# Optimization experiments

Measured on AMD Instinct MI355X. Metric: run time of the kernel, lower is better.

The kernel has to match this reference:

```python
import jax, jax.numpy as jnp
import numpy as np

N_NODES = 10000
N_EDGES = 100000
IN_CH = 64
EDGE_DIM = 16
HID = 128
HEADS = 4
LAYERS = 4
NUM_GRAPHS = 256


def setup_inputs() -> dict:
    key = jax.random.key(0)
    ks = jax.random.split(key, 16)
    s = 0.1
    HC = HEADS * HID
    L = LAYERS
    return {
        "x": jax.random.normal(ks[0], (N_NODES, IN_CH), jnp.float32),
        "edge_index": jax.random.randint(ks[1], (2, N_EDGES), 0, N_NODES, dtype=jnp.int32),
        "edge_attr": jax.random.normal(ks[2], (N_EDGES, EDGE_DIM), jnp.float32),
        "batch": jnp.sort(jax.random.randint(ks[3], (N_NODES,), 0, NUM_GRAPHS, dtype=jnp.int32)),
        "Win": jax.random.normal(ks[4], (IN_CH, HID), jnp.float32) * s,
        "b_in": jnp.zeros((HID,), jnp.float32),
        "Wl": jax.random.normal(ks[5], (L, HID, HC), jnp.float32) * s,
        "bl": jnp.zeros((L, HC), jnp.float32),
        "Wr": jax.random.normal(ks[6], (L, HID, HC), jnp.float32) * s,
        "br": jnp.zeros((L, HC), jnp.float32),
        "We": jax.random.normal(ks[7], (L, EDGE_DIM, HC), jnp.float32) * s,
        "att": jax.random.normal(ks[8], (L, HEADS, HID), jnp.float32) * s,
        "b_gat": jnp.zeros((L, HID), jnp.float32),
        "gamma": jnp.ones((L, HID), jnp.float32),
        "beta": jnp.zeros((L, HID), jnp.float32),
        "Wres": jax.random.normal(ks[9], (L - 1, HID, HID), jnp.float32) * s,
        "bres": jnp.zeros((L - 1, HID), jnp.float32),
        "W1": jax.random.normal(ks[10], (HID, HID), jnp.float32) * s,
        "b1": jnp.zeros((HID,), jnp.float32),
        "W2": jax.random.normal(ks[11], (HID, HID // 2), jnp.float32) * s,
        "b2": jnp.zeros((HID // 2,), jnp.float32),
        "W3": jax.random.normal(ks[12], (HID // 2, 1), jnp.float32) * s,
        "b3": jnp.zeros((1,), jnp.float32),
    }


def _layer_norm(x, g, b):
    mu = x.mean(-1, keepdims=True)
    var = ((x - mu) ** 2).mean(-1, keepdims=True)
    return g * (x - mu) / jnp.sqrt(var + 1e-5) + b


def _gatv2(h, src, dst, edge_attr, Wl, bl, Wr, br, We, att, bias):
    # GATv2Conv, concat=False, share_weights=False, negative_slope=0.2, eval mode
    N = h.shape[0]
    H, C = att.shape
    xl = (h @ Wl + bl).reshape(N, H, C)   # source-side features (lin_l)
    xr = (h @ Wr + br).reshape(N, H, C)   # target-side features (lin_r)
    e = (edge_attr @ We).reshape(-1, H, C)
    m = xl[src] + xr[dst] + e             # [E, H, C]
    m = jnp.where(m > 0, m, 0.2 * m)      # leaky_relu
    logits = jnp.einsum('ehc,hc->eh', m, att)
    lmax = jax.lax.stop_gradient(jax.ops.segment_max(logits, dst, num_segments=N))
    p = jnp.exp(logits - lmax[dst])
    denom = jax.ops.segment_sum(p, dst, num_segments=N)
    alpha = p / (denom[dst] + 1e-16)      # segment softmax over in-edges of each target
    out = jax.ops.segment_sum(alpha[:, :, None] * xl[src], dst, num_segments=N)
    return out.mean(axis=1) + bias        # concat=False -> head mean, plus bias


def reference(x, edge_index, edge_attr, batch, Win, b_in, Wl, bl, Wr, br, We, att,
              b_gat, gamma, beta, Wres, bres, W1, b1, W2, b2, W3, b3):
    src, dst = edge_index[0], edge_index[1]
    h = jax.nn.elu(x @ Win + b_in)
    for i in range(LAYERS):
        h_res = h
        h = _gatv2(h, src, dst, edge_attr, Wl[i], bl[i], Wr[i], br[i], We[i], att[i], b_gat[i])
        h = jax.nn.elu(_layer_norm(h, gamma[i], beta[i]))
        if i > 0:
            h = h + (h_res @ Wres[i - 1] + bres[i - 1])
    sums = jax.ops.segment_sum(h, batch, num_segments=NUM_GRAPHS)
    counts = jax.ops.segment_sum(jnp.ones((h.shape[0], 1), h.dtype), batch, num_segments=NUM_GRAPHS)
    hg = sums / jnp.maximum(counts, 1.0)  # global_mean_pool
    z = jax.nn.relu(hg @ W1 + b1)
    z = jax.nn.relu(z @ W2 + b2)
    return (z @ W3 + b3).reshape(-1)
```

## Files before the change

kernel.cpp:

```cpp
#include <hip/hip_runtime.h>

#define N_NODES 10000
#define N_EDGES 100000
#define IN_CH 64
#define EDGE_DIM 16
#define HID 128
#define HEADS 4
#define HC 512
#define LAYERS 4
#define NUM_GRAPHS 256
#define NCAT 1152
#define LDP 136

typedef __bf16 bf16;
typedef __bf16 bf16x8 __attribute__((ext_vector_type(8)));
typedef __bf16 bf16x4 __attribute__((ext_vector_type(4)));
typedef float floatx4 __attribute__((ext_vector_type(4)));
typedef _Float16 f16;
typedef _Float16 f16x2 __attribute__((ext_vector_type(2)));

__device__ __forceinline__ float elu_f(float x) { return x > 0.f ? x : (__expf(x) - 1.f); }

__global__ __launch_bounds__(128) void k_prep_w(
    const float* __restrict__ Wl, const float* __restrict__ bl,
    const float* __restrict__ Wr, const float* __restrict__ br,
    const float* __restrict__ Wres, const float* __restrict__ bres,
    const float* __restrict__ We,
    bf16* __restrict__ WT, float* __restrict__ bcat, f16* __restrict__ WeH) {
    __shared__ float tile[16][129];
    int nt = blockIdx.x, i = blockIdx.y, z = blockIdx.z;
    int t = threadIdx.x;
    if (nt == 9) {
        if (z < 4) {
            int c = z * 128 + t;
            const float* src = We + (size_t)i * EDGE_DIM * HC + c;
            f16 buf[16];
#pragma unroll
            for (int k = 0; k < EDGE_DIM; k++) buf[k] = (f16)src[(size_t)k * HC];
            f16* dst = WeH + ((size_t)i * HC + c) * EDGE_DIM;
            *(uint4*)dst = *(uint4*)buf;
            *(uint4*)(dst + 8) = *(uint4*)(buf + 8);
        }
        return;
    }
    int n0 = nt * 128;
    const float* base = nullptr; const float* bsrc = nullptr; int ld = 0;
    if (nt < 4)       { base = Wl + (size_t)i * HID * HC + n0;            bsrc = bl + i * HC + n0;              ld = HC; }
    else if (nt < 8)  { base = Wr + (size_t)i * HID * HC + (n0 - 512);    bsrc = br + i * HC + (n0 - 512);      ld = HC; }
    else if (i > 0)   { base = Wres + (size_t)(i - 1) * HID * HID;        bsrc = bres + (size_t)(i - 1) * HID;  ld = HID; }
    if (base) {
#pragma unroll
        for (int r = 0; r < 16; r++) tile[r][t] = base[(size_t)(z * 16 + r) * ld + t];
    } else {
#pragma unroll
        for (int r = 0; r < 16; r++) tile[r][t] = 0.f;
    }
    __syncthreads();
    int n = n0 + t;
    if (z == 0) bcat[(size_t)i * NCAT + n] = base ? bsrc[t] : 0.f;
    bf16* dst = WT + ((size_t)i * NCAT + n) * HID + z * 16;
#pragma unroll
    for (int kc = 0; kc < 2; kc++) {
        bf16x8 v;
#pragma unroll
        for (int u = 0; u < 8; u++) v[u] = (bf16)tile[kc * 8 + u][t];
        *(bf16x8*)(dst + kc * 8) = v;
    }
}

__global__ __launch_bounds__(128) void k_init_h(const float* __restrict__ x,
                                                const float* __restrict__ Win,
                                                const float* __restrict__ b_in,
                                                bf16* __restrict__ h_bf) {
    __shared__ float xs[IN_CH];
    int n = blockIdx.x, t = threadIdx.x;
    if (t < IN_CH) xs[t] = x[(size_t)n * IN_CH + t];
    __syncthreads();
    float s = b_in[t];
#pragma unroll 8
    for (int k = 0; k < IN_CH; k++) s = fmaf(xs[k], Win[k * HID + t], s);
    h_bf[(size_t)n * HID + t] = (bf16)elu_f(s);
}

__global__ __launch_bounds__(256, 2) void k_gemm_mfma(
    const bf16* __restrict__ A, const bf16* __restrict__ WT,
    const float* __restrict__ bcat, bf16* __restrict__ C, int M) {
    __shared__ __align__(16) unsigned short As[128 * LDP];
    __shared__ __align__(16) unsigned short Bs[128 * LDP];
    int t = threadIdx.x;
    int r0 = blockIdx.x * 128, c0 = blockIdx.y * 128;
#pragma unroll
    for (int i = 0; i < 8; i++) {
        int idx = t + i * 256;
        int row = idx >> 4;
        int ch = idx & 15;
        int r = r0 + row; if (r >= M) r = M - 1;
        uint4 va = *(const uint4*)(A + (size_t)r * HID + ch * 8);
        *(uint4*)&As[row * LDP + ch * 8] = va;
        uint4 vb = *(const uint4*)(WT + (size_t)(c0 + row) * HID + ch * 8);
        *(uint4*)&Bs[row * LDP + ch * 8] = vb;
    }
    __syncthreads();

    int wave = t >> 6, lane = t & 63;
    int wm = wave & 1, wn = wave >> 1;
    int quad = lane >> 4, lm = lane & 15;
    floatx4 zero = {0.f, 0.f, 0.f, 0.f};
    floatx4 acc[4][4];
#pragma unroll
    for (int mi = 0; mi < 4; mi++)
#pragma unroll
        for (int ni = 0; ni < 4; ni++) acc[mi][ni] = zero;

    const unsigned short* Ab = &As[(wm * 64 + lm) * LDP + quad * 8];
    const unsigned short* Bb = &Bs[(wn * 64 + lm) * LDP + quad * 8];
#pragma unroll
    for (int ks = 0; ks < 4; ks++) {
        bf16x8 af[4], bfr[4];
#pragma unroll
        for (int mi = 0; mi < 4; mi++) af[mi] = *(const bf16x8*)(Ab + mi * 16 * LDP + ks * 32);
#pragma unroll
        for (int ni = 0; ni < 4; ni++) bfr[ni] = *(const bf16x8*)(Bb + ni * 16 * LDP + ks * 32);
#pragma unroll
        for (int mi = 0; mi < 4; mi++)
#pragma unroll
            for (int ni = 0; ni < 4; ni++)
                acc[mi][ni] = __builtin_amdgcn_mfma_f32_16x16x32_bf16(bfr[ni], af[mi], acc[mi][ni], 0, 0, 0);
    }

#pragma unroll
    for (int mi = 0; mi < 4; mi++) {
        int row = r0 + wm * 64 + mi * 16 + lm;
        if (row < M) {
            bf16* crow = C + (size_t)row * NCAT;
#pragma unroll
            for (int ni = 0; ni < 4; ni++) {
                int cb = c0 + wn * 64 + ni * 16 + quad * 4;
                float4 b4 = *(const float4*)(bcat + cb);
                floatx4 v = acc[mi][ni];
                bf16x4 o = {(bf16)(v[0] + b4.x), (bf16)(v[1] + b4.y),
                            (bf16)(v[2] + b4.z), (bf16)(v[3] + b4.w)};
                *(bf16x4*)(crow + cb) = o;
            }
        }
    }
}

__global__ void k_degree(const int* __restrict__ ei, const int* __restrict__ batch,
                         int* __restrict__ deg, int* __restrict__ cnt) {
    int e = blockIdx.x * blockDim.x + threadIdx.x;
    if (e < N_EDGES) atomicAdd(&deg[ei[N_EDGES + e]], 1);
    if (e < N_NODES) atomicAdd(&cnt[batch[e]], 1);
}

__global__ __launch_bounds__(1024) void k_scan(const int* __restrict__ deg,
                                               int* __restrict__ row_start,
                                               int* __restrict__ cursor) {
    __shared__ int wsum[16];
    __shared__ int carry_s;
    int t = threadIdx.x;
    int wave = t >> 6, lane = t & 63;
    if (t == 0) { carry_s = 0; row_start[0] = 0; }
    __syncthreads();
    for (int base = 0; base < N_NODES; base += 4096) {
        int i0 = base + t * 4;
        int v[4];
#pragma unroll
        for (int u = 0; u < 4; u++) v[u] = (i0 + u < N_NODES) ? deg[i0 + u] : 0;
        int tsum = v[0] + v[1] + v[2] + v[3];
        int incl = tsum;
#pragma unroll
        for (int off = 1; off < 64; off <<= 1) {
            int u = __shfl_up(incl, off, 64);
            if (lane >= off) incl += u;
        }
        if (lane == 63) wsum[wave] = incl;
        __syncthreads();
        if (wave == 0) {
            int ws = (lane < 16) ? wsum[lane] : 0;
#pragma unroll
            for (int off = 1; off < 16; off <<= 1) {
                int u = __shfl_up(ws, off, 64);
                if (lane >= off) ws += u;
            }
            if (lane < 16) wsum[lane] = ws;
        }
        __syncthreads();
        int carry = carry_s;
        int chunk_total = wsum[15];
        int p = carry + ((wave == 0) ? 0 : wsum[wave - 1]) + incl - tsum;
#pragma unroll
        for (int u = 0; u < 4; u++) {
            int i = i0 + u;
            if (i < N_NODES) { cursor[i] = p; p += v[u]; row_start[i + 1] = p; }
        }
        __syncthreads();
        if (t == 0) carry_s = carry + chunk_total;
    }
}

__global__ void k_scatter(const int* __restrict__ ei, const float* __restrict__ edge_attr,
                          int* __restrict__ cursor,
                          int* __restrict__ ssrc, f16* __restrict__ ea_h) {
    int e = blockIdx.x * blockDim.x + threadIdx.x;
    if (e < N_EDGES) {
        int d = ei[N_EDGES + e];
        int pos = atomicAdd(&cursor[d], 1);
        ssrc[pos] = ei[e];
        const float* s = edge_attr + (size_t)e * EDGE_DIM;
        f16 buf[16];
#pragma unroll
        for (int q = 0; q < 16; q++) buf[q] = (f16)s[q];
        f16* dst = ea_h + (size_t)pos * EDGE_DIM;
        *(uint4*)dst = *(uint4*)buf;
        *(uint4*)(dst + 8) = *(uint4*)(buf + 8);
    }
}

__global__ __launch_bounds__(128) void k_edge_fused(
    const bf16* __restrict__ xlr, const f16* __restrict__ ea_h,
    const int* __restrict__ row_start, const int* __restrict__ ssrc,
    const f16* __restrict__ WeH_l, const float* __restrict__ att_l,
    const float* __restrict__ bgat_l, const float* __restrict__ gamma_l,
    const float* __restrict__ beta_l,
    int has_res,
    const int* __restrict__ batch, float* __restrict__ hsum, int do_pool,
    bf16* __restrict__ hbf_out) {
    int n = blockIdx.x;
    int t = threadIdx.x;
    int wave = t >> 6;
    int lane = t & 63;
    int c0 = wave * 256 + lane * 4;
    int head = c0 >> 7;

    const f16x2* wr = (const f16x2*)(WeH_l + (size_t)c0 * EDGE_DIM);
    float4 att4 = *(const float4*)(att_l + head * HID + (c0 & 127));
    bf16x4 vr = *(const bf16x4*)(xlr + (size_t)n * NCAT + 512 + c0);
    float xr0 = (float)vr[0], xr1 = (float)vr[1], xr2 = (float)vr[2], xr3 = (float)vr[3];

    int e0 = row_start[n], e1 = row_start[n + 1];
    float lsum = 0.f;
    float4 acc = {0.f, 0.f, 0.f, 0.f};

    for (int j = e0; j < e1; j++) {
        int s = ssrc[j];
        const f16x2* eah = (const f16x2*)(ea_h + (size_t)j * EDGE_DIM);
        f16x2 ep[8];
#pragma unroll
        for (int kp = 0; kp < 8; kp++) ep[kp] = eah[kp];
        bf16x4 vl = *(const bf16x4*)(xlr + (size_t)s * NCAT + c0);
        float xl0 = (float)vl[0], xl1 = (float)vl[1];
        float xl2 = (float)vl[2], xl3 = (float)vl[3];
        float ec0 = 0.f, ec1 = 0.f, ec2 = 0.f, ec3 = 0.f;
#pragma unroll
        for (int kp = 0; kp < 8; kp++) {
            ec0 = __builtin_amdgcn_fdot2(wr[kp],      ep[kp], ec0, false);
            ec1 = __builtin_amdgcn_fdot2(wr[8 + kp],  ep[kp], ec1, false);
            ec2 = __builtin_amdgcn_fdot2(wr[16 + kp], ep[kp], ec2, false);
            ec3 = __builtin_amdgcn_fdot2(wr[24 + kp], ep[kp], ec3, false);
        }
        float m0 = xl0 + xr0 + ec0; m0 = fmaxf(m0, 0.2f * m0);
        float m1 = xl1 + xr1 + ec1; m1 = fmaxf(m1, 0.2f * m1);
        float m2 = xl2 + xr2 + ec2; m2 = fmaxf(m2, 0.2f * m2);
        float m3 = xl3 + xr3 + ec3; m3 = fmaxf(m3, 0.2f * m3);
        float partial = m0 * att4.x + m1 * att4.y + m2 * att4.z + m3 * att4.w;
#pragma unroll
        for (int off = 1; off < 32; off <<= 1) partial += __shfl_xor(partial, off, 64);
        float p = __expf(partial);
        lsum += p;
        acc.x = fmaf(p, xl0, acc.x);
        acc.y = fmaf(p, xl1, acc.y);
        acc.z = fmaf(p, xl2, acc.z);
        acc.w = fmaf(p, xl3, acc.w);
    }

    float inv = 1.f / (lsum + 1e-16f);

    __shared__ float sout[HC];
    __shared__ float red[4];
    sout[c0 + 0] = acc.x * inv;
    sout[c0 + 1] = acc.y * inv;
    sout[c0 + 2] = acc.z * inv;
    sout[c0 + 3] = acc.w * inv;
    __syncthreads();

    int c = t;
    float v = 0.25f * (sout[c] + sout[c + 128] + sout[c + 256] + sout[c + 384]) + bgat_l[c];
    float s1 = v, s2 = v * v;
#pragma unroll
    for (int off = 1; off < 64; off <<= 1) {
        s1 += __shfl_xor(s1, off, 64);
        s2 += __shfl_xor(s2, off, 64);
    }
    if (lane == 0) { red[wave * 2] = s1; red[wave * 2 + 1] = s2; }
    __syncthreads();
    s1 = red[0] + red[2];
    s2 = red[1] + red[3];
    float mu = s1 * (1.f / HID);
    float var = s2 * (1.f / HID) - mu * mu;
    float rstd = rsqrtf(var + 1e-5f);
    float y = fmaf(gamma_l[c] * (v - mu), rstd, beta_l[c]);
    y = elu_f(y);
    if (has_res) y += (float)xlr[(size_t)n * NCAT + 1024 + c];
    if (do_pool) atomicAdd(&hsum[(size_t)batch[n] * HID + c], y);
    else hbf_out[(size_t)n * HID + c] = (bf16)y;
}

__global__ __launch_bounds__(128) void k_mlp(const float* __restrict__ hsum,
                                             const int* __restrict__ cnt,
                                             const float* __restrict__ W1, const float* __restrict__ b1,
                                             const float* __restrict__ W2, const float* __restrict__ b2,
                                             const float* __restrict__ W3, const float* __restrict__ b3,
                                             float* __restrict__ out) {
    int g = blockIdx.x, t = threadIdx.x;
    __shared__ float hg[HID], z1[HID], z2[64];
    float invc = 1.f / fmaxf((float)cnt[g], 1.f);
    hg[t] = hsum[(size_t)g * HID + t] * invc;
    __syncthreads();
    float s = b1[t];
#pragma unroll 8
    for (int k = 0; k < HID; k++) s = fmaf(hg[k], W1[k * HID + t], s);
    z1[t] = fmaxf(s, 0.f);
    __syncthreads();
    if (t < 64) {
        float s2 = b2[t];
#pragma unroll 8
        for (int k = 0; k < HID; k++) s2 = fmaf(z1[k], W2[k * 64 + t], s2);
        z2[t] = fmaxf(s2, 0.f);
    }
    __syncthreads();
    if (t < 64) {
        float s3 = z2[t] * W3[t];
#pragma unroll
        for (int off = 1; off < 64; off <<= 1) s3 += __shfl_xor(s3, off, 64);
        if (t == 0) out[g] = s3 + b3[0];
    }
}

extern "C" void kernel_launch(void* const* d_in, const int* in_sizes, int n_in,
                              void* d_out, int out_size, void* d_ws, size_t ws_size,
                              hipStream_t stream) {
    const float* x         = (const float*)d_in[0];
    const int*   ei        = (const int*)  d_in[1];
    const float* edge_attr = (const float*)d_in[2];
    const int*   batch     = (const int*)  d_in[3];
    const float* Win       = (const float*)d_in[4];
    const float* b_in      = (const float*)d_in[5];
    const float* Wl        = (const float*)d_in[6];
    const float* bl        = (const float*)d_in[7];
    const float* Wr        = (const float*)d_in[8];
    const float* br        = (const float*)d_in[9];
    const float* We        = (const float*)d_in[10];
    const float* att       = (const float*)d_in[11];
    const float* b_gat     = (const float*)d_in[12];
    const float* gamma     = (const float*)d_in[13];
    const float* beta      = (const float*)d_in[14];
    const float* Wres      = (const float*)d_in[15];
    const float* bres      = (const float*)d_in[16];
    const float* W1        = (const float*)d_in[17];
    const float* b1        = (const float*)d_in[18];
    const float* W2        = (const float*)d_in[19];
    const float* b2        = (const float*)d_in[20];
    const float* W3        = (const float*)d_in[21];
    const float* b3        = (const float*)d_in[22];
    float* out = (float*)d_out;

    char* ws = (char*)d_ws;
    size_t off = 0;
    auto alloc = [&](size_t bytes) -> void* {
        void* p = ws + off;
        off = (off + bytes + 255) & ~(size_t)255;
        return p;
    };
    bf16*  h_bf    = (bf16*) alloc((size_t)N_NODES * HID * 2);
    bf16*  xlr     = (bf16*) alloc((size_t)N_NODES * NCAT * 2);
    bf16*  WT      = (bf16*) alloc((size_t)LAYERS * NCAT * HID * 2);
    float* bcat    = (float*)alloc((size_t)LAYERS * NCAT * 4);
    f16*   WeH     = (f16*)  alloc((size_t)LAYERS * HC * EDGE_DIM * 2);
    f16*   ea_h    = (f16*)  alloc((size_t)N_EDGES * EDGE_DIM * 2);
    char*  zbase   = ws + off;
    float* hsum    = (float*)alloc((size_t)NUM_GRAPHS * HID * 4);
    int*   cnt     = (int*)  alloc((size_t)NUM_GRAPHS * 4);
    int*   deg     = (int*)  alloc((size_t)N_NODES * 4);
    size_t zlen    = (size_t)((ws + off) - zbase);
    int*   rowst   = (int*)  alloc((size_t)(N_NODES + 1) * 4);
    int*   cursor  = (int*)  alloc((size_t)N_NODES * 4);
    int*   ssrc    = (int*)  alloc((size_t)N_EDGES * 4);
    (void)ws_size;

    hipMemsetAsync(zbase, 0, zlen, stream);

    k_prep_w<<<dim3(10, LAYERS, 8), 128, 0, stream>>>(Wl, bl, Wr, br, Wres, bres, We,
                                                      WT, bcat, WeH);
    k_degree<<<(N_EDGES + 255) / 256, 256, 0, stream>>>(ei, batch, deg, cnt);
    k_scan<<<1, 1024, 0, stream>>>(deg, rowst, cursor);
    k_scatter<<<(N_EDGES + 255) / 256, 256, 0, stream>>>(ei, edge_attr, cursor, ssrc, ea_h);
    k_init_h<<<N_NODES, 128, 0, stream>>>(x, Win, b_in, h_bf);

    const int MG = (N_NODES + 127) / 128;
    for (int i = 0; i < LAYERS; i++) {
        int ntiles = (i > 0) ? (NCAT / 128) : (1024 / 128);
        k_gemm_mfma<<<dim3(MG, ntiles), 256, 0, stream>>>(
            h_bf, WT + (size_t)i * NCAT * HID, bcat + (size_t)i * NCAT, xlr, N_NODES);
        k_edge_fused<<<N_NODES, 128, 0, stream>>>(
            xlr, ea_h, rowst, ssrc,
            WeH + (size_t)i * HC * EDGE_DIM, att + (size_t)i * HEADS * HID,
            b_gat + (size_t)i * HID, gamma + (size_t)i * HID, beta + (size_t)i * HID,
            (i > 0) ? 1 : 0,
            batch, hsum, (i == LAYERS - 1) ? 1 : 0, h_bf);
    }

    k_mlp<<<NUM_GRAPHS, 128, 0, stream>>>(hsum, cnt, W1, b1, W2, b2, W3, b3, out);
}
```

Before: 419.5 us.

## Merge prep kernels, split GEMM K staging, unroll edge loop by two

Three setup kernels (weight prep, degree counting, input projection) are merged into one launch that dispatches on block index, removing two kernel launches. The MFMA GEMM now stages K in two 64-wide halves, halving shared memory so more blocks can fit per CU, at the cost of an extra barrier pair. The edge aggregation loop handles two edges per iteration with independent accumulators to expose more memory-level parallelism for the gathers, plus a one-edge tail.

```diff
diff --git a/kernel.cpp b/kernel.cpp
--- a/kernel.cpp
+++ b/kernel.cpp
@@ -10,7 +10,10 @@
 #define LAYERS 4
 #define NUM_GRAPHS 256
 #define NCAT 1152
-#define LDP 136
+#define LDPK 72
+
+#define PREP_BLOCKS 320
+#define DEG_BLOCKS 782
 
 typedef __bf16 bf16;
 typedef __bf16 bf16x8 __attribute__((ext_vector_type(8)));
@@ -21,86 +24,82 @@
 
 __device__ __forceinline__ float elu_f(float x) { return x > 0.f ? x : (__expf(x) - 1.f); }
 
-__global__ __launch_bounds__(128) void k_prep_w(
+__global__ __launch_bounds__(128) void k_prep_all(
     const float* __restrict__ Wl, const float* __restrict__ bl,
     const float* __restrict__ Wr, const float* __restrict__ br,
     const float* __restrict__ Wres, const float* __restrict__ bres,
     const float* __restrict__ We,
-    bf16* __restrict__ WT, float* __restrict__ bcat, f16* __restrict__ WeH) {
-    __shared__ float tile[16][129];
-    int nt = blockIdx.x, i = blockIdx.y, z = blockIdx.z;
+    bf16* __restrict__ WT, float* __restrict__ bcat, f16* __restrict__ WeH,
+    const int* __restrict__ ei, const int* __restrict__ batch,
+    int* __restrict__ deg, int* __restrict__ cnt,
+    const float* __restrict__ x, const float* __restrict__ Win,
+    const float* __restrict__ b_in, bf16* __restrict__ h_bf) {
+    __shared__ float smem[16 * 129];
+    int b = blockIdx.x;
     int t = threadIdx.x;
-    if (nt == 9) {
-        if (z < 4) {
-            int c = z * 128 + t;
-            const float* src = We + (size_t)i * EDGE_DIM * HC + c;
-            f16 buf[16];
-#pragma unroll
-            for (int k = 0; k < EDGE_DIM; k++) buf[k] = (f16)src[(size_t)k * HC];
-            f16* dst = WeH + ((size_t)i * HC + c) * EDGE_DIM;
-            *(uint4*)dst = *(uint4*)buf;
-            *(uint4*)(dst + 8) = *(uint4*)(buf + 8);
-        }
-        return;
-    }
-    int n0 = nt * 128;
-    const float* base = nullptr; const float* bsrc = nullptr; int ld = 0;
-    if (nt < 4)       { base = Wl + (size_t)i * HID * HC + n0;            bsrc = bl + i * HC + n0;              ld = HC; }
-    else if (nt < 8)  { base = Wr + (size_t)i * HID * HC + (n0 - 512);    bsrc = br + i * HC + (n0 - 512);      ld = HC; }
-    else if (i > 0)   { base = Wres + (size_t)(i - 1) * HID * HID;        bsrc = bres + (size_t)(i - 1) * HID;  ld = HID; }
-    if (base) {
-#pragma unroll
-        for (int r = 0; r < 16; r++) tile[r][t] = base[(size_t)(z * 16 + r) * ld + t];
+
+    if (b < PREP_BLOCKS) {
+        int nt = b % 10, i = (b / 10) % LAYERS, z = b / 40;
+        if (nt == 9) {
+            if (z < 4) {
+                int c = z * 128 + t;
+                const float* src = We + (size_t)i * EDGE_DIM * HC + c;
+                f16 buf[16];
+#pragma unroll
+                for (int k = 0; k < EDGE_DIM; k++) buf[k] = (f16)src[(size_t)k * HC];
+                f16* dst = WeH + ((size_t)i * HC + c) * EDGE_DIM;
+                *(uint4*)dst = *(uint4*)buf;
+                *(uint4*)(dst + 8) = *(uint4*)(buf + 8);
+            }
+            return;
+        }
+        float (*tile)[129] = (float(*)[129])smem;
+        int n0 = nt * 128;
+        const float* base = nullptr; const float* bsrc = nullptr; int ld = 0;
+        if (nt < 4)       { base = Wl + (size_t)i * HID * HC + n0;          bsrc = bl + i * HC + n0;              ld = HC; }
+        else if (nt < 8)  { base = Wr + (size_t)i * HID * HC + (n0 - 512);  bsrc = br + i * HC + (n0 - 512);      ld = HC; }
+        else if (i > 0)   { base = Wres + (size_t)(i - 1) * HID * HID;      bsrc = bres + (size_t)(i - 1) * HID;  ld = HID; }
+        if (base) {
+#pragma unroll
+            for (int r = 0; r < 16; r++) tile[r][t] = base[(size_t)(z * 16 + r) * ld + t];
+        } else {
+#pragma unroll
+            for (int r = 0; r < 16; r++) tile[r][t] = 0.f;
+        }
+        __syncthreads();
+        int n = n0 + t;
+        if (z == 0) bcat[(size_t)i * NCAT + n] = base ? bsrc[t] : 0.f;
+        bf16* dst = WT + ((size_t)i * NCAT + n) * HID + z * 16;
+#pragma unroll
+        for (int kc = 0; kc < 2; kc++) {
+            bf16x8 v;
+#pragma unroll
+            for (int u = 0; u < 8; u++) v[u] = (bf16)tile[kc * 8 + u][t];
+            *(bf16x8*)(dst + kc * 8) = v;
+        }
+    } else if (b < PREP_BLOCKS + DEG_BLOCKS) {
+        int e = (b - PREP_BLOCKS) * 128 + t;
+        if (e < N_EDGES) atomicAdd(&deg[ei[N_EDGES + e]], 1);
+        if (e < N_NODES) atomicAdd(&cnt[batch[e]], 1);
     } else {
-#pragma unroll
-        for (int r = 0; r < 16; r++) tile[r][t] = 0.f;
-    }
-    __syncthreads();
-    int n = n0 + t;
-    if (z == 0) bcat[(size_t)i * NCAT + n] = base ? bsrc[t] : 0.f;
-    bf16* dst = WT + ((size_t)i * NCAT + n) * HID + z * 16;
-#pragma unroll
-    for (int kc = 0; kc < 2; kc++) {
-        bf16x8 v;
-#pragma unroll
-        for (int u = 0; u < 8; u++) v[u] = (bf16)tile[kc * 8 + u][t];
-        *(bf16x8*)(dst + kc * 8) = v;
-    }
-}
-
-__global__ __launch_bounds__(128) void k_init_h(const float* __restrict__ x,
-                                                const float* __restrict__ Win,
-                                                const float* __restrict__ b_in,
-                                                bf16* __restrict__ h_bf) {
-    __shared__ float xs[IN_CH];
-    int n = blockIdx.x, t = threadIdx.x;
-    if (t < IN_CH) xs[t] = x[(size_t)n * IN_CH + t];
-    __syncthreads();
-    float s = b_in[t];
+        int n = b - (PREP_BLOCKS + DEG_BLOCKS);
+        float* xs = smem;
+        if (t < IN_CH) xs[t] = x[(size_t)n * IN_CH + t];
+        __syncthreads();
+        float s = b_in[t];
 #pragma unroll 8
-    for (int k = 0; k < IN_CH; k++) s = fmaf(xs[k], Win[k * HID + t], s);
-    h_bf[(size_t)n * HID + t] = (bf16)elu_f(s);
-}
-
-__global__ __launch_bounds__(256, 2) void k_gemm_mfma(
+        for (int k = 0; k < IN_CH; k++) s = fmaf(xs[k], Win[k * HID + t], s);
+        h_bf[(size_t)n * HID + t] = (bf16)elu_f(s);
+    }
+}
+
+__global__ __launch_bounds__(256) void k_gemm_mfma(
     const bf16* __restrict__ A, const bf16* __restrict__ WT,
     const float* __restrict__ bcat, bf16* __restrict__ C, int M) {
-    __shared__ __align__(16) unsigned short As[128 * LDP];
-    __shared__ __align__(16) unsigned short Bs[128 * LDP];
+    __shared__ __align__(16) unsigned short As[128 * LDPK];
+    __shared__ __align__(16) unsigned short Bs[128 * LDPK];
     int t = threadIdx.x;
     int r0 = blockIdx.x * 128, c0 = blockIdx.y * 128;
-#pragma unroll
-    for (int i = 0; i < 8; i++) {
-        int idx = t + i * 256;
-        int row = idx >> 4;
-        int ch = idx & 15;
-        int r = r0 + row; if (r >= M) r = M - 1;
-        uint4 va = *(const uint4*)(A + (size_t)r * HID + ch * 8);
-        *(uint4*)&As[row * LDP + ch * 8] = va;
-        uint4 vb = *(const uint4*)(WT + (size_t)(c0 + row) * HID + ch * 8);
-        *(uint4*)&Bs[row * LDP + ch * 8] = vb;
-    }
-    __syncthreads();
 
     int wave = t >> 6, lane = t & 63;
     int wm = wave & 1, wn = wave >> 1;
@@ -112,20 +111,36 @@
 #pragma unroll
         for (int ni = 0; ni < 4; ni++) acc[mi][ni] = zero;
 
-    const unsigned short* Ab = &As[(wm * 64 + lm) * LDP + quad * 8];
-    const unsigned short* Bb = &Bs[(wn * 64 + lm) * LDP + quad * 8];
-#pragma unroll
-    for (int ks = 0; ks < 4; ks++) {
-        bf16x8 af[4], bfr[4];
-#pragma unroll
-        for (int mi = 0; mi < 4; mi++) af[mi] = *(const bf16x8*)(Ab + mi * 16 * LDP + ks * 32);
-#pragma unroll
-        for (int ni = 0; ni < 4; ni++) bfr[ni] = *(const bf16x8*)(Bb + ni * 16 * LDP + ks * 32);
-#pragma unroll
-        for (int mi = 0; mi < 4; mi++)
-#pragma unroll
-            for (int ni = 0; ni < 4; ni++)
-                acc[mi][ni] = __builtin_amdgcn_mfma_f32_16x16x32_bf16(bfr[ni], af[mi], acc[mi][ni], 0, 0, 0);
+    const unsigned short* Ab = &As[(wm * 64 + lm) * LDPK + quad * 8];
+    const unsigned short* Bb = &Bs[(wn * 64 + lm) * LDPK + quad * 8];
+
+    for (int kc = 0; kc < 2; kc++) {
+#pragma unroll
+        for (int i = 0; i < 4; i++) {
+            int idx = t + i * 256;
+            int row = idx >> 3;
+            int ch = idx & 7;
+            int r = r0 + row; if (r >= M) r = M - 1;
+            *(uint4*)&As[row * LDPK + ch * 8] =
+                *(const uint4*)(A + (size_t)r * HID + kc * 64 + ch * 8);
+            *(uint4*)&Bs[row * LDPK + ch * 8] =
+                *(const uint4*)(WT + (size_t)(c0 + row) * HID + kc * 64 + ch * 8);
+        }
+        __syncthreads();
+#pragma unroll
+        for (int ks = 0; ks < 2; ks++) {
+            bf16x8 af[4], bfr[4];
+#pragma unroll
+            for (int mi = 0; mi < 4; mi++) af[mi] = *(const bf16x8*)(Ab + mi * 16 * LDPK + ks * 32);
+#pragma unroll
+            for (int ni = 0; ni < 4; ni++) bfr[ni] = *(const bf16x8*)(Bb + ni * 16 * LDPK + ks * 32);
+#pragma unroll
+            for (int mi = 0; mi < 4; mi++)
+#pragma unroll
+                for (int ni = 0; ni < 4; ni++)
+                    acc[mi][ni] = __builtin_amdgcn_mfma_f32_16x16x32_bf16(bfr[ni], af[mi], acc[mi][ni], 0, 0, 0);
+        }
+        __syncthreads();
     }
 
 #pragma unroll
@@ -144,13 +159,6 @@
             }
         }
     }
-}
-
-__global__ void k_degree(const int* __restrict__ ei, const int* __restrict__ batch,
-                         int* __restrict__ deg, int* __restrict__ cnt) {
-    int e = blockIdx.x * blockDim.x + threadIdx.x;
-    if (e < N_EDGES) atomicAdd(&deg[ei[N_EDGES + e]], 1);
-    if (e < N_NODES) atomicAdd(&cnt[batch[e]], 1);
 }
 
 __global__ __launch_bounds__(1024) void k_scan(const int* __restrict__ deg,
@@ -239,49 +247,96 @@
     float xr0 = (float)vr[0], xr1 = (float)vr[1], xr2 = (float)vr[2], xr3 = (float)vr[3];
 
     int e0 = row_start[n], e1 = row_start[n + 1];
-    float lsum = 0.f;
-    float4 acc = {0.f, 0.f, 0.f, 0.f};
-
-    for (int j = e0; j < e1; j++) {
-        int s = ssrc[j];
+    float l0 = 0.f, l1 = 0.f;
+    float4 a0 = {0.f, 0.f, 0.f, 0.f}, a1 = {0.f, 0.f, 0.f, 0.f};
+
+    int j = e0;
+    for (; j + 1 < e1; j += 2) {
+        int s0 = ssrc[j], s1 = ssrc[j + 1];
         const f16x2* eah = (const f16x2*)(ea_h + (size_t)j * EDGE_DIM);
-        f16x2 ep[8];
-#pragma unroll
-        for (int kp = 0; kp < 8; kp++) ep[kp] = eah[kp];
-        bf16x4 vl = *(const bf16x4*)(xlr + (size_t)s * NCAT + c0);
-        float xl0 = (float)vl[0], xl1 = (float)vl[1];
-        float xl2 = (float)vl[2], xl3 = (float)vl[3];
-        float ec0 = 0.f, ec1 = 0.f, ec2 = 0.f, ec3 = 0.f;
+        f16x2 ep0[8], ep1[8];
+#pragma unroll
+        for (int kp = 0; kp < 8; kp++) ep0[kp] = eah[kp];
+#pragma unroll
+        for (int kp = 0; kp < 8; kp++) ep1[kp] = eah[8 + kp];
+        bf16x4 vl0 = *(const bf16x4*)(xlr + (size_t)s0 * NCAT + c0);
+        bf16x4 vl1 = *(const bf16x4*)(xlr + (size_t)s1 * NCAT + c0);
+
+        float p0c0 = 0.f, p0c1 = 0.f, p0c2 = 0.f, p0c3 = 0.f;
+        float p1c0 = 0.f, p1c1 = 0.f, p1c2 = 0.f, p1c3 = 0.f;
 #pragma unroll
         for (int kp = 0; kp < 8; kp++) {
-            ec0 = __builtin_amdgcn_fdot2(wr[kp],      ep[kp], ec0, false);
-            ec1 = __builtin_amdgcn_fdot2(wr[8 + kp],  ep[kp], ec1, false);
-            ec2 = __builtin_amdgcn_fdot2(wr[16 + kp], ep[kp], ec2, false);
-            ec3 = __builtin_amdgcn_fdot2(wr[24 + kp], ep[kp], ec3, false);
-        }
-        float m0 = xl0 + xr0 + ec0; m0 = fmaxf(m0, 0.2f * m0);
-        float m1 = xl1 + xr1 + ec1; m1 = fmaxf(m1, 0.2f * m1);
-        float m2 = xl2 + xr2 + ec2; m2 = fmaxf(m2, 0.2f * m2);
-        float m3 = xl3 + xr3 + ec3; m3 = fmaxf(m3, 0.2f * m3);
-        float partial = m0 * att4.x + m1 * att4.y + m2 * att4.z + m3 * att4.w;
-#pragma unroll
-        for (int off = 1; off < 32; off <<= 1) partial += __shfl_xor(partial, off, 64);
-        float p = __expf(partial);
-        lsum += p;
-        acc.x = fmaf(p, xl0, acc.x);
-        acc.y = fmaf(p, xl1, acc.y);
-        acc.z = fmaf(p, xl2, acc.z);
-        acc.w = fmaf(p, xl3, acc.w);
-    }
-
-    float inv = 1.f / (lsum + 1e-16f);
+            p0c0 = __builtin_amdgcn_fdot2(wr[kp],      ep0[kp], p0c0, false);
+            p1c0 = __builtin_amdgcn_fdot2(wr[kp],      ep1[kp], p1c0, false);
+            p0c1 = __builtin_amdgcn_fdot2(wr[8 + kp],  ep0[kp], p0c1, false);
+            p1c1 = __builtin_amdgcn_fdot2(wr[8 + kp],  ep1[kp], p1c1, false);
+            p0c2 = __builtin_amdgcn_fdot2(wr[16 + kp], ep0[kp], p0c2, false);
+            p1c2 = __builtin_amdgcn_fdot2(wr[16 + kp], ep1[kp], p1c2, false);
+            p0c3 = __builtin_amdgcn_fdot2(wr[24 + kp], ep0[kp], p0c3, false);
+            p1c3 = __builtin_amdgcn_fdot2(wr[24 + kp], ep1[kp], p1c3, false);
+        }
+        float x00 = (float)vl0[0], x01 = (float)vl0[1], x02 = (float)vl0[2], x03 = (float)vl0[3];
+        float x10 = (float)vl1[0], x11 = (float)vl1[1], x12 = (float)vl1[2], x13 = (float)vl1[3];
+        float m00 = x00 + xr0 + p0c0; m00 = fmaxf(m00, 0.2f * m00);
+        float m01 = x01 + xr1 + p0c1; m01 = fmaxf(m01, 0.2f * m01);
+        float m02 = x02 + xr2 + p0c2; m02 = fmaxf(m02, 0.2f * m02);
+        float m03 = x03 + xr3 + p0c3; m03 = fmaxf(m03, 0.2f * m03);
+        float m10 = x10 + xr0 + p1c0; m10 = fmaxf(m10, 0.2f * m10);
+        float m11 = x11 + xr1 + p1c1; m11 = fmaxf(m11, 0.2f * m11);
+        float m12 = x12 + xr2 + p1c2; m12 = fmaxf(m12, 0.2f * m12);
+        float m13 = x13 + xr3 + p1c3; m13 = fmaxf(m13, 0.2f * m13);
+        float part0 = m00 * att4.x + m01 * att4.y + m02 * att4.z + m03 * att4.w;
+        float part1 = m10 * att4.x + m11 * att4.y + m12 * att4.z + m13 * att4.w;
+#pragma unroll
+        for (int off = 1; off < 32; off <<= 1) {
+            part0 += __shfl_xor(part0, off, 64);
+            part1 += __shfl_xor(part1, off, 64);
+        }
+        float p0 = __expf(part0);
+        float p1 = __expf(part1);
+        l0 += p0; l1 += p1;
+        a0.x = fmaf(p0, x00, a0.x); a0.y = fmaf(p0, x01, a0.y);
+        a0.z = fmaf(p0, x02, a0.z); a0.w = fmaf(p0, x03, a0.w);
+        a1.x = fmaf(p1, x10, a1.x); a1.y = fmaf(p1, x11, a1.y);
+        a1.z = fmaf(p1, x12, a1.z); a1.w = fmaf(p1, x13, a1.w);
+    }
+    if (j < e1) {
+        int s0 = ssrc[j];
+        const f16x2* eah = (const f16x2*)(ea_h + (size_t)j * EDGE_DIM);
+        f16x2 ep0[8];
+#pragma unroll
+        for (int kp = 0; kp < 8; kp++) ep0[kp] = eah[kp];
+        bf16x4 vl0 = *(const bf16x4*)(xlr + (size_t)s0 * NCAT + c0);
+        float p0c0 = 0.f, p0c1 = 0.f, p0c2 = 0.f, p0c3 = 0.f;
+#pragma unroll
+        for (int kp = 0; kp < 8; kp++) {
+            p0c0 = __builtin_amdgcn_fdot2(wr[kp],      ep0[kp], p0c0, false);
+            p0c1 = __builtin_amdgcn_fdot2(wr[8 + kp],  ep0[kp], p0c1, false);
+            p0c2 = __builtin_amdgcn_fdot2(wr[16 + kp], ep0[kp], p0c2, false);
+            p0c3 = __builtin_amdgcn_fdot2(wr[24 + kp], ep0[kp], p0c3, false);
+        }
+        float x00 = (float)vl0[0], x01 = (float)vl0[1], x02 = (float)vl0[2], x03 = (float)vl0[3];
+        float m00 = x00 + xr0 + p0c0; m00 = fmaxf(m00, 0.2f * m00);
+        float m01 = x01 + xr1 + p0c1; m01 = fmaxf(m01, 0.2f * m01);
+        float m02 = x02 + xr2 + p0c2; m02 = fmaxf(m02, 0.2f * m02);
+        float m03 = x03 + xr3 + p0c3; m03 = fmaxf(m03, 0.2f * m03);
+        float part0 = m00 * att4.x + m01 * att4.y + m02 * att4.z + m03 * att4.w;
+#pragma unroll
+        for (int off = 1; off < 32; off <<= 1) part0 += __shfl_xor(part0, off, 64);
+        float p0 = __expf(part0);
+        l0 += p0;
+        a0.x = fmaf(p0, x00, a0.x); a0.y = fmaf(p0, x01, a0.y);
+        a0.z = fmaf(p0, x02, a0.z); a0.w = fmaf(p0, x03, a0.w);
+    }
+
+    float inv = 1.f / (l0 + l1 + 1e-16f);
 
     __shared__ float sout[HC];
     __shared__ float red[4];
-    sout[c0 + 0] = acc.x * inv;
-    sout[c0 + 1] = acc.y * inv;
-    sout[c0 + 2] = acc.z * inv;
-    sout[c0 + 3] = acc.w * inv;
+    sout[c0 + 0] = (a0.x + a1.x) * inv;
+    sout[c0 + 1] = (a0.y + a1.y) * inv;
+    sout[c0 + 2] = (a0.z + a1.z) * inv;
+    sout[c0 + 3] = (a0.w + a1.w) * inv;
     __syncthreads();
 
     int c = t;
@@ -390,12 +445,11 @@
 
     hipMemsetAsync(zbase, 0, zlen, stream);
 
-    k_prep_w<<<dim3(10, LAYERS, 8), 128, 0, stream>>>(Wl, bl, Wr, br, Wres, bres, We,
-                                                      WT, bcat, WeH);
-    k_degree<<<(N_EDGES + 255) / 256, 256, 0, stream>>>(ei, batch, deg, cnt);
+    k_prep_all<<<PREP_BLOCKS + DEG_BLOCKS + N_NODES, 128, 0, stream>>>(
+        Wl, bl, Wr, br, Wres, bres, We, WT, bcat, WeH,
+        ei, batch, deg, cnt, x, Win, b_in, h_bf);
     k_scan<<<1, 1024, 0, stream>>>(deg, rowst, cursor);
     k_scatter<<<(N_EDGES + 255) / 256, 256, 0, stream>>>(ei, edge_attr, cursor, ssrc, ea_h);
-    k_init_h<<<N_NODES, 128, 0, stream>>>(x, Win, b_in, h_bf);
 
     const int MG = (N_NODES + 127) / 128;
     for (int i = 0; i < LAYERS; i++) {
```

New measurement: 409.1 us. 2.5% less time.
